# Optimization experiments

Measured on AMD Instinct MI355X. Metric: run time of the kernel, lower is better.

Reference implementation:

```python
import jax, jax.numpy as jnp
import numpy as np

MARGIN = 0.1
N = 64  # ranking list length (labels.shape[1])
# all pairs (i, j) with i < j, matching itertools.combinations(range(N), 2)
_I, _J = np.triu_indices(N, k=1)  # each [P], P = N*(N-1)/2


def setup_inputs() -> dict:
    key = jax.random.key(0)
    k1, k2 = jax.random.split(key)
    scores = jax.random.normal(k1, (32768, N), dtype=jnp.float32)
    labels = jax.random.normal(k2, (32768, N), dtype=jnp.float32)
    return {"scores": scores, "labels": labels}


def reference(scores, labels):
    # indx = labels.argsort(); scores gathered at sorted positions
    indx = jnp.argsort(labels, axis=1)                      # [B, N]
    s = jnp.take_along_axis(scores, indx, axis=1)           # [B, N]
    i_idx = jnp.asarray(_I)
    j_idx = jnp.asarray(_J)
    # combinations give i < j, so target y = -1 always:
    # per-pair loss = mean_b max(0, -y*(x1 - x2) + margin*|i-j|)
    #               = mean_b max(0, (s_i - s_j) + margin*(j - i))
    diff = s[:, i_idx] - s[:, j_idx]                        # [B, P]
    marg = (MARGIN * (j_idx - i_idx)).astype(scores.dtype)  # [P]
    per_pair = jnp.mean(jnp.maximum(diff + marg, 0.0), axis=0)  # [P]
    loss = jnp.sum(per_pair)
    return loss.reshape(1)  # torch version returns shape [1]
```

## Files before the change

### kernel.cpp

```cpp
#include <hip/hip_runtime.h>

#define N 64
#define MARGIN 0.1f
#define WAVES_PER_BLOCK 4

__global__ __launch_bounds__(256) void mmrl_kernel(const float* __restrict__ scores,
                                                   const float* __restrict__ labels,
                                                   float* __restrict__ out,
                                                   int rows) {
    const int lane = threadIdx.x & 63;
    const int w    = threadIdx.x >> 6;
    const int gwave = blockIdx.x * WAVES_PER_BLOCK + w;
    const int nwaves = gridDim.x * WAVES_PER_BLOCK;

    float acc = 0.0f;

    for (int row = gwave; row < rows; row += nwaves) {
        const int rbase = __builtin_amdgcn_readfirstlane(row) * N;
        const float labv = labels[rbase + lane];
        const float scv  = scores[rbase + lane];

        int pa = 0, pb = 0;
        #pragma unroll
        for (int e = 0; e < N; e += 2) {
            const float le0 = labels[rbase + e];
            const float le1 = labels[rbase + e + 1];
            pa += (le0 < labv) ? 1 : 0;
            pb += (le1 < labv) ? 1 : 0;
        }
        const int pv = pa + pb;

        const float u = fmaf(-MARGIN, (float)pv, scv);
        const int ubits = __float_as_int(u);

        int qa = 0, qb = 0;
        #pragma unroll
        for (int e = 0; e < N; e += 2) {
            const float u0 = __int_as_float(__builtin_amdgcn_readlane(ubits, e));
            const float u1 = __int_as_float(__builtin_amdgcn_readlane(ubits, e + 1));
            qa += (u0 < u) ? 1 : 0;
            qb += (u1 < u) ? 1 : 0;
        }
        const int qv = qa + qb;

        acc = fmaf(u, (float)(qv - pv), acc);
    }

    #pragma unroll
    for (int off = 32; off > 0; off >>= 1)
        acc += __shfl_down(acc, off, 64);

    __shared__ float wsum[WAVES_PER_BLOCK];
    if (lane == 0) wsum[w] = acc;
    __syncthreads();
    if (threadIdx.x == 0) {
        float s = 0.0f;
        #pragma unroll
        for (int i = 0; i < WAVES_PER_BLOCK; ++i) s += wsum[i];
        atomicAdd(out, s * (1.0f / (float)rows));
    }
}

extern "C" void kernel_launch(void* const* d_in, const int* in_sizes, int n_in,
                              void* d_out, int out_size, void* d_ws, size_t ws_size,
                              hipStream_t stream) {
    const float* scores = (const float*)d_in[0];
    const float* labels = (const float*)d_in[1];
    float* out = (float*)d_out;
    const int rows = in_sizes[0] / N;

    (void)hipMemsetAsync(out, 0, sizeof(float), stream);

    mmrl_kernel<<<2048, 256, 0, stream>>>(scores, labels, out, rows);
}
```

Baseline: 94.36 us.

## Process two rows per wave with float4 label loads and two-pass reduction

Each wave now handles two rows per iteration, so the independent rank-counting chains interleave and give more instruction-level parallelism. The 64 label broadcasts are read as uniform float4 loads instead of scalar loads. The memset plus per-block atomicAdd is replaced by per-block partial sums written to the workspace and a second single-block reduction kernel. This adds a second launch and relies on the workspace being large enough for the partials.

```diff
diff --git a/kernel.cpp b/kernel.cpp
--- a/kernel.cpp
+++ b/kernel.cpp
@@ -3,11 +3,12 @@
 #define N 64
 #define MARGIN 0.1f
 #define WAVES_PER_BLOCK 4
+#define NBLOCKS 2048
 
-__global__ __launch_bounds__(256) void mmrl_kernel(const float* __restrict__ scores,
-                                                   const float* __restrict__ labels,
-                                                   float* __restrict__ out,
-                                                   int rows) {
+__global__ __launch_bounds__(256) void mmrl_partial(const float* __restrict__ scores,
+                                                    const float* __restrict__ labels,
+                                                    float* __restrict__ partial,
+                                                    int rows) {
     const int lane = threadIdx.x & 63;
     const int w    = threadIdx.x >> 6;
     const int gwave = blockIdx.x * WAVES_PER_BLOCK + w;
@@ -15,35 +16,55 @@
 
     float acc = 0.0f;
 
-    for (int row = gwave; row < rows; row += nwaves) {
-        const int rbase = __builtin_amdgcn_readfirstlane(row) * N;
-        const float labv = labels[rbase + lane];
-        const float scv  = scores[rbase + lane];
+    for (int row0 = gwave * 2; row0 < rows; row0 += nwaves * 2) {
+        const int rA = row0;
+        const int rB = (row0 + 1 < rows) ? row0 + 1 : row0;
+        const int baseA = __builtin_amdgcn_readfirstlane(rA) * N;
+        const int baseB = __builtin_amdgcn_readfirstlane(rB) * N;
 
-        int pa = 0, pb = 0;
+        const float labA = labels[baseA + lane];
+        const float labB = labels[baseB + lane];
+        const float scA  = scores[baseA + lane];
+        const float scB  = scores[baseB + lane];
+
+        const float4* A4 = (const float4*)(labels + baseA);
+        const float4* B4 = (const float4*)(labels + baseB);
+        int pA0 = 0, pA1 = 0, pB0 = 0, pB1 = 0;
+        #pragma unroll
+        for (int kk = 0; kk < N / 4; ++kk) {
+            const float4 a = A4[kk];
+            const float4 b = B4[kk];
+            pA0 += (a.x < labA) + (a.z < labA);
+            pA1 += (a.y < labA) + (a.w < labA);
+            pB0 += (b.x < labB) + (b.z < labB);
+            pB1 += (b.y < labB) + (b.w < labB);
+        }
+        const int pA = pA0 + pA1;
+        const int pB = pB0 + pB1;
+
+        const float uA = fmaf(-MARGIN, (float)pA, scA);
+        const float uB = fmaf(-MARGIN, (float)pB, scB);
+        const int uAb = __float_as_int(uA);
+        const int uBb = __float_as_int(uB);
+
+        int qA0 = 0, qA1 = 0, qB0 = 0, qB1 = 0;
         #pragma unroll
         for (int e = 0; e < N; e += 2) {
-            const float le0 = labels[rbase + e];
-            const float le1 = labels[rbase + e + 1];
-            pa += (le0 < labv) ? 1 : 0;
-            pb += (le1 < labv) ? 1 : 0;
+            const float a0 = __int_as_float(__builtin_amdgcn_readlane(uAb, e));
+            const float a1 = __int_as_float(__builtin_amdgcn_readlane(uAb, e + 1));
+            const float b0 = __int_as_float(__builtin_amdgcn_readlane(uBb, e));
+            const float b1 = __int_as_float(__builtin_amdgcn_readlane(uBb, e + 1));
+            qA0 += (a0 < uA);
+            qA1 += (a1 < uA);
+            qB0 += (b0 < uB);
+            qB1 += (b1 < uB);
         }
-        const int pv = pa + pb;
+        const int qA = qA0 + qA1;
+        const int qB = qB0 + qB1;
 
-        const float u = fmaf(-MARGIN, (float)pv, scv);
-        const int ubits = __float_as_int(u);
-
-        int qa = 0, qb = 0;
-        #pragma unroll
-        for (int e = 0; e < N; e += 2) {
-            const float u0 = __int_as_float(__builtin_amdgcn_readlane(ubits, e));
-            const float u1 = __int_as_float(__builtin_amdgcn_readlane(ubits, e + 1));
-            qa += (u0 < u) ? 1 : 0;
-            qb += (u1 < u) ? 1 : 0;
-        }
-        const int qv = qa + qb;
-
-        acc = fmaf(u, (float)(qv - pv), acc);
+        acc = fmaf(uA, (float)(qA - pA), acc);
+        const float cB = fmaf(uB, (float)(qB - pB), 0.0f);
+        acc += (row0 + 1 < rows) ? cB : 0.0f;
     }
 
     #pragma unroll
@@ -57,8 +78,25 @@
         float s = 0.0f;
         #pragma unroll
         for (int i = 0; i < WAVES_PER_BLOCK; ++i) s += wsum[i];
-        atomicAdd(out, s * (1.0f / (float)rows));
+        partial[blockIdx.x] = s;
     }
+}
+
+__global__ __launch_bounds__(256) void mmrl_reduce(const float* __restrict__ partial,
+                                                   float* __restrict__ out,
+                                                   int npartial, float inv_rows) {
+    const int t = threadIdx.x;
+    float s = 0.0f;
+    for (int i = t; i < npartial; i += 256)
+        s += partial[i];
+    #pragma unroll
+    for (int off = 32; off > 0; off >>= 1)
+        s += __shfl_down(s, off, 64);
+    __shared__ float wsum[4];
+    if ((t & 63) == 0) wsum[t >> 6] = s;
+    __syncthreads();
+    if (t == 0)
+        out[0] = (wsum[0] + wsum[1] + wsum[2] + wsum[3]) * inv_rows;
 }
 
 extern "C" void kernel_launch(void* const* d_in, const int* in_sizes, int n_in,
@@ -67,9 +105,9 @@
     const float* scores = (const float*)d_in[0];
     const float* labels = (const float*)d_in[1];
     float* out = (float*)d_out;
+    float* partial = (float*)d_ws;
     const int rows = in_sizes[0] / N;
 
-    (void)hipMemsetAsync(out, 0, sizeof(float), stream);
-
-    mmrl_kernel<<<2048, 256, 0, stream>>>(scores, labels, out, rows);
+    mmrl_partial<<<NBLOCKS, 256, 0, stream>>>(scores, labels, partial, rows);
+    mmrl_reduce<<<1, 256, 0, stream>>>(partial, out, NBLOCKS, 1.0f / (float)rows);
 }
```

New measurement: 87.52 us. -7.2%, faster.
